# Kernel optimization log

Hardware: AMD Instinct MI355X
Metric: run time of the kernel (lower is better)

The kernel has to match this reference:

```python
import jax, jax.numpy as jnp
import numpy as np

BATCH, NVIS, NHID, NCOND = 4096, 1024, 4096, 512


def setup_inputs() -> dict:
    key = jax.random.key(0)
    ks = jax.random.split(key, 6)
    return {
        "visible_data": jax.random.uniform(ks[0], (BATCH, NVIS), dtype=jnp.float32),
        "cond_data": jax.random.normal(ks[1], (BATCH, NCOND), dtype=jnp.float32),
        # uniform noise replaces torch.bernoulli's internal RNG: sample = (noise < p)
        "noise": jax.random.uniform(ks[2], (BATCH, NHID), dtype=jnp.float32),
        "W": jax.random.normal(ks[3], (NVIS, NHID), dtype=jnp.float32) * 0.1,
        "b": jnp.zeros((1, NVIS), dtype=jnp.float32),
        "c": jnp.zeros((1, NHID), dtype=jnp.float32),
        "A": jax.random.normal(ks[4], (NCOND, NVIS), dtype=jnp.float32) * 0.1,
        "B": jax.random.normal(ks[5], (NCOND, NHID), dtype=jnp.float32) * 0.1,
    }


def reference(visible_data, cond_data, noise, W, b, c, A, B):
    # sample_h_given_vu: sigmoid(v@W + u@B + c), bernoulli sample via uniform noise
    h1_mean = jax.nn.sigmoid(visible_data @ W + cond_data @ B + c)  # [B, nhid]
    h1_sample = (noise < h1_mean).astype(h1_mean.dtype)
    # sample_v_given_hu (binary): L1-normalized exp == softmax, then argmax one-hot
    pre = h1_sample @ W.T + cond_data @ A + b  # [B, nvis]
    v1_mean = jax.nn.softmax(pre, axis=1)
    max_idx = jnp.argmax(v1_mean, axis=1)
    v1_sample = jax.nn.one_hot(max_idx, pre.shape[1], dtype=pre.dtype)
    return v1_sample
```

## Files before the change

kernel.cpp:

```cpp
#include <hip/hip_runtime.h>
#include <math.h>

static constexpr int BATCH = 4096;
static constexpr int NVIS  = 1024;
static constexpr int NHID  = 4096;
static constexpr int NCOND = 512;

typedef __attribute__((ext_vector_type(8))) short bf16x8;
typedef __attribute__((ext_vector_type(4))) float f32x4;

static constexpr unsigned HCAP = 131072;
static constexpr unsigned RCAP = 256;
static constexpr size_t MB = 1u << 20;

static constexpr size_t F_WT0   = 0;
static constexpr size_t F_WT1   = F_WT0  + 8*MB;
static constexpr size_t F_BMT0  = F_WT1  + 8*MB;
static constexpr size_t F_BMT1  = F_BMT0 + 4*MB;
static constexpr size_t F_AT0   = F_BMT1 + 4*MB;
static constexpr size_t F_AT1   = F_AT0  + 1*MB;
static constexpr size_t F_V0    = F_AT1  + 1*MB;
static constexpr size_t F_V1    = F_V0   + 8*MB;
static constexpr size_t F_U0    = F_V1   + 8*MB;
static constexpr size_t F_U1    = F_U0   + 4*MB;
static constexpr size_t F_WR0   = F_U1   + 4*MB;
static constexpr size_t F_WR1   = F_WR0  + 8*MB;
static constexpr size_t F_H     = F_WR1  + 8*MB;
static constexpr size_t F_BB    = F_H    + 32*MB;
static constexpr size_t F_HFLAG = F_BB   + 1*MB;
static constexpr size_t F_RFLAG = F_HFLAG + 512*1024;
static constexpr size_t F_RBEST = F_RFLAG + 16384;
static constexpr size_t F_CNT   = F_RBEST + 16384;
static constexpr size_t F_PREB  = F_CNT  + 256;
static constexpr size_t WS_FULL = F_PREB + 2*MB;

__device__ __forceinline__ void gload16(const void* g, void* l) {
    __builtin_amdgcn_global_load_lds(
        (const __attribute__((address_space(1))) void*)g,
        (__attribute__((address_space(3))) void*)l, 16, 0, 0);
}

__device__ __forceinline__ void split1(float x, unsigned short& hi, unsigned short& lo) {
    unsigned u = __float_as_uint(x);
    unsigned r = u + 0x7FFFu + ((u >> 16) & 1u);
    hi = (unsigned short)(r >> 16);
    float rem = x - __uint_as_float(r & 0xFFFF0000u);
    unsigned u2 = __float_as_uint(rem);
    unsigned r2 = u2 + 0x7FFFu + ((u2 >> 16) & 1u);
    lo = (unsigned short)(r2 >> 16);
}

__device__ __forceinline__ void merge3(float& b, unsigned& ix, float& s,
                                       float b2, unsigned i2, float s2) {
    if (b2 > b || (b2 == b && i2 < ix)) { s = fmaxf(b, s2); b = b2; ix = i2; }
    else                                { s = fmaxf(s, b2); }
}

#define SFENCE() __builtin_amdgcn_sched_barrier(0)
#define BARRIER() do { asm volatile("" ::: "memory"); SFENCE(); \
                       __builtin_amdgcn_s_barrier(); SFENCE(); \
                       asm volatile("" ::: "memory"); } while (0)
#define VMW(N) asm volatile("s_waitcnt vmcnt(" #N ")" ::: "memory")
#define LGKM0() do { asm volatile("s_waitcnt lgkmcnt(0)" ::: "memory"); SFENCE(); } while (0)

__global__ void kz_zero(unsigned* c) { if (threadIdx.x < 64) c[threadIdx.x] = 0; }

__global__ __launch_bounds__(256) void transpose_split(
    const float* __restrict__ src, int R, int C,
    unsigned short* __restrict__ d0, unsigned short* __restrict__ d1) {
    __shared__ float tile[32][33];
    const int c0 = blockIdx.x * 32, r0 = blockIdx.y * 32;
    const int tx = threadIdx.x & 31, ty = threadIdx.x >> 5;
#pragma unroll
    for (int e = 0; e < 4; ++e)
        tile[ty + e * 8][tx] = src[(size_t)(r0 + ty + e * 8) * C + c0 + tx];
    __syncthreads();
#pragma unroll
    for (int e = 0; e < 4; ++e) {
        int c = c0 + ty + e * 8;
        unsigned short hi, lo;
        split1(tile[tx][ty + e * 8], hi, lo);
        d0[(size_t)c * R + r0 + tx] = hi;
        d1[(size_t)c * R + r0 + tx] = lo;
    }
}

__global__ __launch_bounds__(256) void transpose_f32(
    const float* __restrict__ src, int R, int C, float* __restrict__ dst) {
    __shared__ float tile[32][33];
    const int c0 = blockIdx.x * 32, r0 = blockIdx.y * 32;
    const int tx = threadIdx.x & 31, ty = threadIdx.x >> 5;
#pragma unroll
    for (int e = 0; e < 4; ++e)
        tile[ty + e * 8][tx] = src[(size_t)(r0 + ty + e * 8) * C + c0 + tx];
    __syncthreads();
#pragma unroll
    for (int e = 0; e < 4; ++e)
        dst[(size_t)(c0 + ty + e * 8) * R + r0 + tx] = tile[tx][ty + e * 8];
}

__global__ __launch_bounds__(256) void split_planes(
    const float* __restrict__ src, int n4,
    unsigned short* __restrict__ p0, unsigned short* __restrict__ p1) {
    for (int i = blockIdx.x * 256 + threadIdx.x; i < n4; i += gridDim.x * 256) {
        float4 v = ((const float4*)src)[i];
        unsigned short h0,h1,h2,h3,l0,l1,l2,l3;
        split1(v.x,h0,l0); split1(v.y,h1,l1); split1(v.z,h2,l2); split1(v.w,h3,l3);
        ((ushort4*)p0)[i] = make_ushort4(h0,h1,h2,h3);
        ((ushort4*)p1)[i] = make_ushort4(l0,l1,l2,l3);
    }
}

__global__ __launch_bounds__(512, 1) void k1_4p(
    const float* __restrict__ noise,
    const unsigned short* __restrict__ V0, const unsigned short* __restrict__ V1,
    const unsigned short* __restrict__ U0, const unsigned short* __restrict__ U1,
    const unsigned short* __restrict__ WT0, const unsigned short* __restrict__ WT1,
    const unsigned short* __restrict__ BmT0, const unsigned short* __restrict__ BmT1,
    const float* __restrict__ cvec, unsigned short* __restrict__ hout,
    unsigned* __restrict__ hcnt, unsigned* __restrict__ hflag)
{
    __shared__ __align__(16) unsigned short As0[2][256][32], As1[2][256][32],
                                            Bs0[2][256][32], Bs1[2][256][32];
    const int t = threadIdx.x, lane = t & 63, wid = t >> 6;
    const int g = lane >> 4, cc = lane & 15;
    const int wrow = wid >> 2, wcol = wid & 3;
    const int pc = (g ^ ((cc >> 1) & 3)) * 8;
    const int nwg = gridDim.x * gridDim.y;
    const int bid = blockIdx.y * gridDim.x + blockIdx.x;
    const int q = nwg >> 3;
    const int swz = (bid & 7) * q + (bid >> 3);
    const int b0 = (swz / gridDim.x) * 256;
    const int j0 = (swz % gridDim.x) * 256;

    auto srcs = [&](int ks, const unsigned short*& A0_, const unsigned short*& A1_,
                    const unsigned short*& B0_, const unsigned short*& B1_,
                    int& K_, int& k0_) {
        if (ks < 32) { A0_ = V0; A1_ = V1; B0_ = WT0; B1_ = WT1; K_ = 1024; k0_ = ks * 32; }
        else         { A0_ = U0; A1_ = U1; B0_ = BmT0; B1_ = BmT1; K_ = 512; k0_ = (ks - 32) * 32; }
    };
    auto stageA = [&](int ks, int bi, int mh) {
        const unsigned short *A0_, *A1_, *B0_, *B1_; int K_, k0_;
        srcs(ks, A0_, A1_, B0_, B1_, K_, k0_);
        int rl = t >> 2, s = t & 3;
        int r = mh * 128 + rl;
        int sc = s ^ ((r >> 1) & 3);
        size_t ga = (size_t)(b0 + r) * K_ + k0_ + sc * 8;
        size_t ldd = (size_t)mh * 4096 + (size_t)t * 8;
        gload16(A0_ + ga, &As0[bi][0][0] + ldd);
        gload16(A1_ + ga, &As1[bi][0][0] + ldd);
    };
    auto stageB = [&](int ks, int bi, int nh) {
        const unsigned short *A0_, *A1_, *B0_, *B1_; int K_, k0_;
        srcs(ks, A0_, A1_, B0_, B1_, K_, k0_);
        int rl = t >> 2, s = t & 3;
        int r = nh * 128 + rl;
        int sc = s ^ ((r >> 1) & 3);
        size_t gb = (size_t)(j0 + r) * K_ + k0_ + sc * 8;
        size_t ldd = (size_t)nh * 4096 + (size_t)t * 8;
        gload16(B0_ + gb, &Bs0[bi][0][0] + ldd);
        gload16(B1_ + gb, &Bs1[bi][0][0] + ldd);
    };

    f32x4 acc[8][4] = {};
    bf16x8 a0q[4], a1q[4];
    bf16x8 b0a[2][2], b1a[2][2];

    auto readA = [&](int cur, int mh) {
#pragma unroll
        for (int k = 0; k < 4; ++k) {
            int r = wrow * 128 + (4 * mh + k) * 16 + cc;
            a0q[k] = *(const bf16x8*)&As0[cur][r][pc];
            a1q[k] = *(const bf16x8*)&As1[cur][r][pc];
        }
    };
    auto readB = [&](int cur, int nh) {
#pragma unroll
        for (int k = 0; k < 2; ++k) {
            int n = wcol * 64 + (2 * nh + k) * 16 + cc;
            b0a[nh][k] = *(const bf16x8*)&Bs0[cur][n][pc];
            b1a[nh][k] = *(const bf16x8*)&Bs1[cur][n][pc];
        }
    };
    auto mfma24 = [&](int mh, int nh) {
#pragma unroll
        for (int k = 0; k < 4; ++k)
#pragma unroll
            for (int n = 0; n < 2; ++n) {
                f32x4 c = acc[4 * mh + k][2 * nh + n];
                c = __builtin_amdgcn_mfma_f32_16x16x32_bf16(a0q[k], b0a[nh][n], c, 0, 0, 0);
                c = __builtin_amdgcn_mfma_f32_16x16x32_bf16(a0q[k], b1a[nh][n], c, 0, 0, 0);
                c = __builtin_amdgcn_mfma_f32_16x16x32_bf16(a1q[k], b0a[nh][n], c, 0, 0, 0);
                acc[4 * mh + k][2 * nh + n] = c;
            }
    };

    stageA(0, 0, 0);
    stageB(0, 0, 0);
    stageB(0, 0, 1);
    stageA(0, 0, 1);
    VMW(4);
    BARRIER();

    for (int tt = 0; tt < 48; ++tt) {
        const int cur = tt & 1, nb = cur ^ 1;
        const bool pre = (tt + 1 < 48);
        readA(cur, 0); readB(cur, 0);
        if (pre) stageA(tt + 1, nb, 0);
        BARRIER();
        LGKM0();
        __builtin_amdgcn_s_setprio(1); mfma24(0, 0); __builtin_amdgcn_s_setprio(0);
        if (pre) { VMW(4); } else { VMW(2); }
        BARRIER();
        readB(cur, 1);
        if (pre) stageB(tt + 1, nb, 0);
        BARRIER();
        LGKM0();
        __builtin_amdgcn_s_setprio(1); mfma24(0, 1); __builtin_amdgcn_s_setprio(0);
        if (pre) { VMW(4); } else { VMW(0); }
        BARRIER();
        readA(cur, 1);
        if (pre) stageB(tt + 1, nb, 1);
        BARRIER();
        LGKM0();
        __builtin_amdgcn_s_setprio(1); mfma24(1, 0); __builtin_amdgcn_s_setprio(0);
        BARRIER();
        if (pre) stageA(tt + 1, nb, 1);
        BARRIER();
        LGKM0();
        __builtin_amdgcn_s_setprio(1); mfma24(1, 1); __builtin_amdgcn_s_setprio(0);
        if (pre) { VMW(4); }
        BARRIER();
    }

#pragma unroll
    for (int ni = 0; ni < 4; ++ni) {
        int j = j0 + wcol * 64 + ni * 16 + cc;
        float cj = cvec[j];
#pragma unroll
        for (int mi = 0; mi < 8; ++mi) {
#pragma unroll
            for (int i = 0; i < 4; ++i) {
                int b = b0 + wrow * 128 + mi * 16 + g * 4 + i;
                float z = acc[mi][ni][i] + cj;
                float m = 1.0f / (1.0f + __expf(-z));
                float nv = noise[(size_t)b * NHID + j];
                hout[(size_t)b * NHID + j] = (nv < m) ? (unsigned short)0x3F80 : (unsigned short)0;
                if (fabsf(nv - m) < 2.5e-4f) {
                    unsigned p = atomicAdd(hcnt, 1u);
                    if (p < HCAP) hflag[p] = ((unsigned)b << 12) | (unsigned)j;
                }
            }
        }
    }
}

__global__ __launch_bounds__(512, 4) void k2_t(
    const unsigned short* __restrict__ hbf,
    const unsigned short* __restrict__ U0, const unsigned short* __restrict__ U1,
    const unsigned short* __restrict__ WR0, const unsigned short* __restrict__ WR1,
    const unsigned short* __restrict__ AT0, const unsigned short* __restrict__ AT1,
    const float* __restrict__ bvec, float4* __restrict__ blockbest)
{
    __shared__ __align__(16) unsigned short As0[128][32], As1[128][32],
                                            Bs0[128][32], Bs1[128][32];
    __shared__ float4 mbuf[4][128];
    const int t = threadIdx.x, lane = t & 63, wid = t >> 6;
    const int g = lane >> 4, cc = lane & 15;
    const int wrow = wid >> 2, wcol = wid & 3;
    const int pc = (g ^ ((cc >> 1) & 3)) * 8;
    const int nwg = gridDim.x * gridDim.y;
    const int bid = blockIdx.y * gridDim.x + blockIdx.x;
    const int q = nwg >> 3;
    const int swz = (bid & 7) * q + (bid >> 3);
    const int b0 = (swz / gridDim.x) * 128;
    const int i0 = (swz % gridDim.x) * 128;

    f32x4 acc[4][2] = {};

    for (int k0 = 0; k0 < NHID; k0 += 32) {
        __syncthreads();
        {
            int r = t >> 2, s = t & 3, sc = s ^ ((r >> 1) & 3);
            gload16(hbf + (size_t)(b0 + r) * NHID + k0 + sc * 8,
                    &As0[0][0] + (size_t)t * 8);
            size_t go = (size_t)(i0 + r) * NHID + k0 + sc * 8;
            gload16(WR0 + go, &Bs0[0][0] + (size_t)t * 8);
            gload16(WR1 + go, &Bs1[0][0] + (size_t)t * 8);
        }
        __syncthreads();
        bf16x8 bb0[2], bb1[2];
#pragma unroll
        for (int ni = 0; ni < 2; ++ni) {
            int n = wcol * 32 + ni * 16 + cc;
            bb0[ni] = *(const bf16x8*)&Bs0[n][pc];
            bb1[ni] = *(const bf16x8*)&Bs1[n][pc];
        }
#pragma unroll
        for (int mi = 0; mi < 4; ++mi) {
            bf16x8 a = *(const bf16x8*)&As0[wrow * 64 + mi * 16 + cc][pc];
#pragma unroll
            for (int ni = 0; ni < 2; ++ni) {
                acc[mi][ni] = __builtin_amdgcn_mfma_f32_16x16x32_bf16(a, bb0[ni], acc[mi][ni], 0, 0, 0);
                acc[mi][ni] = __builtin_amdgcn_mfma_f32_16x16x32_bf16(a, bb1[ni], acc[mi][ni], 0, 0, 0);
            }
        }
    }
    for (int k0 = 0; k0 < NCOND; k0 += 32) {
        __syncthreads();
        {
            int r = t >> 2, s = t & 3, sc = s ^ ((r >> 1) & 3);
            size_t ga = (size_t)(b0 + r) * NCOND + k0 + sc * 8;
            gload16(U0 + ga, &As0[0][0] + (size_t)t * 8);
            gload16(U1 + ga, &As1[0][0] + (size_t)t * 8);
            size_t go = (size_t)(i0 + r) * NCOND + k0 + sc * 8;
            gload16(AT0 + go, &Bs0[0][0] + (size_t)t * 8);
            gload16(AT1 + go, &Bs1[0][0] + (size_t)t * 8);
        }
        __syncthreads();
        bf16x8 bb0[2], bb1[2];
#pragma unroll
        for (int ni = 0; ni < 2; ++ni) {
            int n = wcol * 32 + ni * 16 + cc;
            bb0[ni] = *(const bf16x8*)&Bs0[n][pc];
            bb1[ni] = *(const bf16x8*)&Bs1[n][pc];
        }
#pragma unroll
        for (int mi = 0; mi < 4; ++mi) {
            int r = wrow * 64 + mi * 16 + cc;
            bf16x8 a0 = *(const bf16x8*)&As0[r][pc];
            bf16x8 a1 = *(const bf16x8*)&As1[r][pc];
#pragma unroll
            for (int ni = 0; ni < 2; ++ni) {
                acc[mi][ni] = __builtin_amdgcn_mfma_f32_16x16x32_bf16(a0, bb0[ni], acc[mi][ni], 0, 0, 0);
                acc[mi][ni] = __builtin_amdgcn_mfma_f32_16x16x32_bf16(a0, bb1[ni], acc[mi][ni], 0, 0, 0);
                acc[mi][ni] = __builtin_amdgcn_mfma_f32_16x16x32_bf16(a1, bb0[ni], acc[mi][ni], 0, 0, 0);
            }
        }
    }

#pragma unroll
    for (int ni = 0; ni < 2; ++ni) {
        int colb = i0 + wcol * 32 + ni * 16 + cc;
        float bb = bvec[colb];
#pragma unroll
        for (int mi = 0; mi < 4; ++mi)
#pragma unroll
            for (int i = 0; i < 4; ++i) acc[mi][ni][i] += bb;
    }
#pragma unroll
    for (int mi = 0; mi < 4; ++mi) {
#pragma unroll
        for (int i = 0; i < 4; ++i) {
            float best = acc[mi][0][i];
            unsigned bidx = (unsigned)(i0 + wcol * 32 + cc);
            float sec = -3.4e38f;
            merge3(best, bidx, sec, acc[mi][1][i],
                   (unsigned)(i0 + wcol * 32 + 16 + cc), -3.4e38f);
#pragma unroll
            for (int m = 1; m < 16; m <<= 1) {
                float ob = __shfl_xor(best, m);
                unsigned oi = __shfl_xor(bidx, m);
                float os = __shfl_xor(sec, m);
                merge3(best, bidx, sec, ob, oi, os);
            }
            if (cc == 0)
                mbuf[wcol][wrow * 64 + mi * 16 + g * 4 + i] =
                    make_float4(best, sec, __uint_as_float(bidx), 0.f);
        }
    }
    __syncthreads();
    if (t < 128) {
        float4 f0 = mbuf[0][t];
        float best = f0.x, sec = f0.y;
        unsigned bidx = __float_as_uint(f0.z);
#pragma unroll
        for (int wq = 1; wq < 4; ++wq) {
            float4 fq = mbuf[wq][t];
            merge3(best, bidx, sec, fq.x, __float_as_uint(fq.z), fq.y);
        }
        blockbest[(size_t)(b0 + t) * 8 + (unsigned)(i0 >> 7)] =
            make_float4(best, sec, __uint_as_float(bidx), 0.f);
    }
}

__global__ __launch_bounds__(256) void k5_recheck_h(
    const float* __restrict__ vd, const float* __restrict__ cd, const float* __restrict__ noise,
    const float* __restrict__ WTf, const float* __restrict__ BmTf, const float* __restrict__ cvec,
    const unsigned* __restrict__ hcnt, const unsigned* __restrict__ hflag,
    unsigned short* __restrict__ h) {
    const int gw = (blockIdx.x * 256 + threadIdx.x) >> 6, lane = threadIdx.x & 63;
    const int nw = gridDim.x * 4;
    unsigned n = *hcnt; if (n > HCAP) n = HCAP;
    for (unsigned e = gw; e < n; e += nw) {
        unsigned p = hflag[e];
        int b = p >> 12, j = p & 4095;
        double s = 0.0;
        for (int k = lane; k < NVIS; k += 64)
            s += (double)vd[(size_t)b * NVIS + k] * (double)WTf[(size_t)j * NVIS + k];
        for (int k = lane; k < NCOND; k += 64)
            s += (double)cd[(size_t)b * NCOND + k] * (double)BmTf[(size_t)j * NCOND + k];
        for (int m = 32; m; m >>= 1) s += __shfl_xor(s, m);
        if (lane == 0) {
            double z = s + (double)cvec[j];
            double mm = 1.0 / (1.0 + exp(-z));
            h[(size_t)b * NHID + j] =
                ((double)noise[(size_t)b * NHID + j] < mm) ? (unsigned short)0x3F80 : (unsigned short)0;
        }
    }
}

__global__ __launch_bounds__(256) void k3_merge8(
    const float4* __restrict__ blockbest, unsigned* __restrict__ rowbest,
    unsigned* __restrict__ rcnt, unsigned* __restrict__ rowflag) {
    const int t = threadIdx.x;
    const int row = blockIdx.x * 32 + (t >> 3), e = t & 7;
    float4 f = blockbest[(size_t)row * 8 + e];
    float best = f.x, sec = f.y;
    unsigned idx = __float_as_uint(f.z);
#pragma unroll
    for (int m = 1; m < 8; m <<= 1) {
        float ob = __shfl_xor(best, m);
        unsigned oi = __shfl_xor(idx, m);
        float os = __shfl_xor(sec, m);
        merge3(best, idx, sec, ob, oi, os);
    }
    if (e == 0) {
        rowbest[row] = idx;
        if (best - sec < 1e-3f) {
            unsigned p = atomicAdd(rcnt, 1u);
            if (p < 4096) rowflag[p] = (unsigned)row;
        }
    }
}

__global__ __launch_bounds__(256) void k_onehot(const unsigned* __restrict__ rowbest,
                                                float* __restrict__ out) {
    const int row = blockIdx.x;
    const unsigned idx = rowbest[row];
    const int base = threadIdx.x * 4;
    float4 o;
    o.x = (base + 0 == (int)idx) ? 1.f : 0.f;
    o.y = (base + 1 == (int)idx) ? 1.f : 0.f;
    o.z = (base + 2 == (int)idx) ? 1.f : 0.f;
    o.w = (base + 3 == (int)idx) ? 1.f : 0.f;
    *(float4*)(out + (size_t)row * NVIS + base) = o;
}

__global__ __launch_bounds__(256) void k6_rows_pre(
    const unsigned short* __restrict__ h, const float* __restrict__ cd,
    const float* __restrict__ W, const float* __restrict__ ATf, const float* __restrict__ bvec,
    const unsigned* __restrict__ rcnt, const unsigned* __restrict__ rowflag,
    double* __restrict__ prebuf) {
    const int gw = (blockIdx.x * 256 + threadIdx.x) >> 6, lane = threadIdx.x & 63;
    const int nw = gridDim.x * 4;
    unsigned n = *rcnt; if (n > RCAP) n = RCAP;
    for (unsigned e = gw; e < n * 1024u; e += nw) {
        int ri = e >> 10, i = e & 1023;
        int b = (int)rowflag[ri];
        double s = 0.0;
        for (int k = lane; k < NHID; k += 64) {
            double hv = h[(size_t)b * NHID + k] ? 1.0 : 0.0;
            s += hv * (double)W[(size_t)i * NHID + k];
        }
        for (int k = lane; k < NCOND; k += 64)
            s += (double)cd[(size_t)b * NCOND + k] * (double)ATf[(size_t)i * NCOND + k];
        for (int m = 32; m; m >>= 1) s += __shfl_xor(s, m);
        if (lane == 0) prebuf[(size_t)ri * 1024 + i] = s + (double)bvec[i];
    }
}

__global__ __launch_bounds__(256) void k6_rows_argmax(
    const unsigned* __restrict__ rcnt, const unsigned* __restrict__ rowflag,
    const double* __restrict__ prebuf, float* __restrict__ out) {
    __shared__ double sv[256];
    __shared__ int si[256];
    unsigned n = *rcnt; if (n > RCAP) n = RCAP;
    const int t = threadIdx.x;
    for (unsigned ri = blockIdx.x; ri < n; ri += gridDim.x) {
        const int row = (int)rowflag[ri];
        const double* pr = prebuf + (size_t)ri * 1024;
        double best = pr[t * 4];
        int bi = t * 4;
#pragma unroll
        for (int e = 1; e < 4; ++e) {
            double v = pr[t * 4 + e];
            if (v > best) { best = v; bi = t * 4 + e; }
        }
        sv[t] = best; si[t] = bi;
        __syncthreads();
        for (int s = 128; s; s >>= 1) {
            if (t < s) {
                double v2 = sv[t + s]; int i2 = si[t + s];
                if (v2 > sv[t] || (v2 == sv[t] && i2 < si[t])) { sv[t] = v2; si[t] = i2; }
            }
            __syncthreads();
        }
        const int amax = si[0];
        const int base = t * 4;
        float4 o;
        o.x = (base + 0 == amax) ? 1.f : 0.f;
        o.y = (base + 1 == amax) ? 1.f : 0.f;
        o.z = (base + 2 == amax) ? 1.f : 0.f;
        o.w = (base + 3 == amax) ? 1.f : 0.f;
        *(float4*)(out + (size_t)row * NVIS + base) = o;
        __syncthreads();
    }
}

extern "C" void kernel_launch(void* const* d_in, const int* in_sizes, int n_in,
                              void* d_out, int out_size, void* d_ws, size_t ws_size,
                              hipStream_t stream) {
    const float* vd = (const float*)d_in[0];
    const float* cd = (const float*)d_in[1];
    const float* nz = (const float*)d_in[2];
    const float* W  = (const float*)d_in[3];
    const float* bv = (const float*)d_in[4];
    const float* cv = (const float*)d_in[5];
    const float* Am = (const float*)d_in[6];
    const float* Bm = (const float*)d_in[7];
    float* out = (float*)d_out;
    char* w = (char*)d_ws;

    unsigned short* WT0  = (unsigned short*)(w + F_WT0);
    unsigned short* WT1  = (unsigned short*)(w + F_WT1);
    unsigned short* BmT0 = (unsigned short*)(w + F_BMT0);
    unsigned short* BmT1 = (unsigned short*)(w + F_BMT1);
    unsigned short* AT0  = (unsigned short*)(w + F_AT0);
    unsigned short* AT1  = (unsigned short*)(w + F_AT1);
    unsigned short* V0   = (unsigned short*)(w + F_V0);
    unsigned short* V1   = (unsigned short*)(w + F_V1);
    unsigned short* U0   = (unsigned short*)(w + F_U0);
    unsigned short* U1   = (unsigned short*)(w + F_U1);
    unsigned short* WR0  = (unsigned short*)(w + F_WR0);
    unsigned short* WR1  = (unsigned short*)(w + F_WR1);
    unsigned short* hbf  = (unsigned short*)(w + F_H);
    float4*   blockbest  = (float4*)(w + F_BB);
    unsigned* hflag      = (unsigned*)(w + F_HFLAG);
    unsigned* rowflag    = (unsigned*)(w + F_RFLAG);
    unsigned* rowbest    = (unsigned*)(w + F_RBEST);
    unsigned* counters   = (unsigned*)(w + F_CNT);
    double*   prebuf     = (double*)(w + F_PREB);
    unsigned* hcnt = &counters[0];
    unsigned* rcnt = &counters[1];
    float* WTf32  = (float*)(w + F_V0);
    float* BmTf32 = (float*)(w + F_WT0);
    float* ATf32  = (float*)(w + F_WT1);

    dim3 blk(256);
    kz_zero<<<1, 64, 0, stream>>>(counters);
    transpose_split<<<dim3(NHID / 32, NVIS / 32), blk, 0, stream>>>(W, NVIS, NHID, WT0, WT1);
    transpose_split<<<dim3(NHID / 32, NCOND / 32), blk, 0, stream>>>(Bm, NCOND, NHID, BmT0, BmT1);
    transpose_split<<<dim3(NVIS / 32, NCOND / 32), blk, 0, stream>>>(Am, NCOND, NVIS, AT0, AT1);
    split_planes<<<2048, blk, 0, stream>>>(vd, BATCH * NVIS / 4, V0, V1);
    split_planes<<<2048, blk, 0, stream>>>(cd, BATCH * NCOND / 4, U0, U1);
    split_planes<<<2048, blk, 0, stream>>>(W, NVIS * NHID / 4, WR0, WR1);
    k1_4p<<<dim3(NHID / 256, BATCH / 256), 512, 0, stream>>>(
        nz, V0, V1, U0, U1, WT0, WT1, BmT0, BmT1, cv, hbf, hcnt, hflag);
    transpose_f32<<<dim3(NHID / 32, NVIS / 32), blk, 0, stream>>>(W, NVIS, NHID, WTf32);
    transpose_f32<<<dim3(NHID / 32, NCOND / 32), blk, 0, stream>>>(Bm, NCOND, NHID, BmTf32);
    transpose_f32<<<dim3(NVIS / 32, NCOND / 32), blk, 0, stream>>>(Am, NCOND, NVIS, ATf32);
    k5_recheck_h<<<256, blk, 0, stream>>>(vd, cd, nz, WTf32, BmTf32, cv, hcnt, hflag, hbf);
    k2_t<<<dim3(NVIS / 128, BATCH / 128), 512, 0, stream>>>(
        hbf, U0, U1, WR0, WR1, AT0, AT1, bv, blockbest);
    k3_merge8<<<BATCH / 32, blk, 0, stream>>>(blockbest, rowbest, rcnt, rowflag);
    k_onehot<<<BATCH, blk, 0, stream>>>(rowbest, out);
    k6_rows_pre<<<512, blk, 0, stream>>>(hbf, cd, W, ATf32, bv, rcnt, rowflag, prebuf);
    k6_rows_argmax<<<64, blk, 0, stream>>>(rcnt, rowflag, prebuf, out);
}
```

Measured before the change: 512.6 us.

## Give each k2 wave a 64x64 tile and fuse W row split into transpose

The second GEMM kernel k2 now runs 256 threads per block with 4 waves in a 2x2 layout instead of 8 waves. Each wave computes a 64x64 output tile, doubling its accumulators, so B fragments are reused across more MFMAs and there is less shared-memory read traffic per flop. The W split into row-major bf16 hi/lo planes is folded into the transpose kernel, which removes one full pass over W. The trade-off is more registers per thread and fewer waves per block, which may hurt latency hiding.

```diff
diff --git a/kernel.cpp b/kernel.cpp
--- a/kernel.cpp
+++ b/kernel.cpp
@@ -82,6 +82,34 @@
         split1(tile[tx][ty + e * 8], hi, lo);
         d0[(size_t)c * R + r0 + tx] = hi;
         d1[(size_t)c * R + r0 + tx] = lo;
+    }
+}
+
+__global__ __launch_bounds__(256) void transpose_split_plus(
+    const float* __restrict__ src, int R, int C,
+    unsigned short* __restrict__ dT0, unsigned short* __restrict__ dT1,
+    unsigned short* __restrict__ dR0, unsigned short* __restrict__ dR1) {
+    __shared__ float tile[32][33];
+    const int c0 = blockIdx.x * 32, r0 = blockIdx.y * 32;
+    const int tx = threadIdx.x & 31, ty = threadIdx.x >> 5;
+#pragma unroll
+    for (int e = 0; e < 4; ++e) {
+        int r = r0 + ty + e * 8;
+        float v = src[(size_t)r * C + c0 + tx];
+        tile[ty + e * 8][tx] = v;
+        unsigned short hi, lo;
+        split1(v, hi, lo);
+        dR0[(size_t)r * C + c0 + tx] = hi;
+        dR1[(size_t)r * C + c0 + tx] = lo;
+    }
+    __syncthreads();
+#pragma unroll
+    for (int e = 0; e < 4; ++e) {
+        int c = c0 + ty + e * 8;
+        unsigned short hi, lo;
+        split1(tile[tx][ty + e * 8], hi, lo);
+        dT0[(size_t)c * R + r0 + tx] = hi;
+        dT1[(size_t)c * R + r0 + tx] = lo;
     }
 }
 
@@ -195,10 +223,7 @@
             }
     };
 
-    stageA(0, 0, 0);
-    stageB(0, 0, 0);
-    stageB(0, 0, 1);
-    stageA(0, 0, 1);
+    stageA(0, 0, 0); stageB(0, 0, 0); stageB(0, 0, 1); stageA(0, 0, 1);
     VMW(4);
     BARRIER();
 
@@ -255,7 +280,7 @@
     }
 }
 
-__global__ __launch_bounds__(512, 4) void k2_t(
+__global__ __launch_bounds__(256, 5) void k2_v(
     const unsigned short* __restrict__ hbf,
     const unsigned short* __restrict__ U0, const unsigned short* __restrict__ U1,
     const unsigned short* __restrict__ WR0, const unsigned short* __restrict__ WR1,
@@ -264,10 +289,10 @@
 {
     __shared__ __align__(16) unsigned short As0[128][32], As1[128][32],
                                             Bs0[128][32], Bs1[128][32];
-    __shared__ float4 mbuf[4][128];
+    __shared__ float4 mbuf[2][128];
     const int t = threadIdx.x, lane = t & 63, wid = t >> 6;
     const int g = lane >> 4, cc = lane & 15;
-    const int wrow = wid >> 2, wcol = wid & 3;
+    const int wrow = wid >> 1, wcol = wid & 1;
     const int pc = (g ^ ((cc >> 1) & 3)) * 8;
     const int nwg = gridDim.x * gridDim.y;
     const int bid = blockIdx.y * gridDim.x + blockIdx.x;
@@ -276,23 +301,28 @@
     const int b0 = (swz / gridDim.x) * 128;
     const int i0 = (swz % gridDim.x) * 128;
 
-    f32x4 acc[4][2] = {};
+    f32x4 acc[4][4] = {};
 
     for (int k0 = 0; k0 < NHID; k0 += 32) {
         __syncthreads();
         {
-            int r = t >> 2, s = t & 3, sc = s ^ ((r >> 1) & 3);
+            int r = t >> 1, s = t & 1;
+        }
+#pragma unroll
+        for (int e = 0; e < 2; ++e) {
+            int idx = t + e * 256, r = idx >> 2, s = idx & 3;
+            int sc = s ^ ((r >> 1) & 3);
             gload16(hbf + (size_t)(b0 + r) * NHID + k0 + sc * 8,
-                    &As0[0][0] + (size_t)t * 8);
+                    &As0[0][0] + (size_t)idx * 8);
             size_t go = (size_t)(i0 + r) * NHID + k0 + sc * 8;
-            gload16(WR0 + go, &Bs0[0][0] + (size_t)t * 8);
-            gload16(WR1 + go, &Bs1[0][0] + (size_t)t * 8);
+            gload16(WR0 + go, &Bs0[0][0] + (size_t)idx * 8);
+            gload16(WR1 + go, &Bs1[0][0] + (size_t)idx * 8);
         }
         __syncthreads();
-        bf16x8 bb0[2], bb1[2];
-#pragma unroll
-        for (int ni = 0; ni < 2; ++ni) {
-            int n = wcol * 32 + ni * 16 + cc;
+        bf16x8 bb0[4], bb1[4];
+#pragma unroll
+        for (int ni = 0; ni < 4; ++ni) {
+            int n = wcol * 64 + ni * 16 + cc;
             bb0[ni] = *(const bf16x8*)&Bs0[n][pc];
             bb1[ni] = *(const bf16x8*)&Bs1[n][pc];
         }
@@ -300,7 +330,7 @@
         for (int mi = 0; mi < 4; ++mi) {
             bf16x8 a = *(const bf16x8*)&As0[wrow * 64 + mi * 16 + cc][pc];
 #pragma unroll
-            for (int ni = 0; ni < 2; ++ni) {
+            for (int ni = 0; ni < 4; ++ni) {
                 acc[mi][ni] = __builtin_amdgcn_mfma_f32_16x16x32_bf16(a, bb0[ni], acc[mi][ni], 0, 0, 0);
                 acc[mi][ni] = __builtin_amdgcn_mfma_f32_16x16x32_bf16(a, bb1[ni], acc[mi][ni], 0, 0, 0);
             }
@@ -308,20 +338,22 @@
     }
     for (int k0 = 0; k0 < NCOND; k0 += 32) {
         __syncthreads();
-        {
-            int r = t >> 2, s = t & 3, sc = s ^ ((r >> 1) & 3);
+#pragma unroll
+        for (int e = 0; e < 2; ++e) {
+            int idx = t + e * 256, r = idx >> 2, s = idx & 3;
+            int sc = s ^ ((r >> 1) & 3);
             size_t ga = (size_t)(b0 + r) * NCOND + k0 + sc * 8;
-            gload16(U0 + ga, &As0[0][0] + (size_t)t * 8);
-            gload16(U1 + ga, &As1[0][0] + (size_t)t * 8);
+            gload16(U0 + ga, &As0[0][0] + (size_t)idx * 8);
+            gload16(U1 + ga, &As1[0][0] + (size_t)idx * 8);
             size_t go = (size_t)(i0 + r) * NCOND + k0 + sc * 8;
-            gload16(AT0 + go, &Bs0[0][0] + (size_t)t * 8);
-            gload16(AT1 + go, &Bs1[0][0] + (size_t)t * 8);
+            gload16(AT0 + go, &Bs0[0][0] + (size_t)idx * 8);
+            gload16(AT1 + go, &Bs1[0][0] + (size_t)idx * 8);
         }
         __syncthreads();
-        bf16x8 bb0[2], bb1[2];
-#pragma unroll
-        for (int ni = 0; ni < 2; ++ni) {
-            int n = wcol * 32 + ni * 16 + cc;
+        bf16x8 bb0[4], bb1[4];
+#pragma unroll
+        for (int ni = 0; ni < 4; ++ni) {
+            int n = wcol * 64 + ni * 16 + cc;
             bb0[ni] = *(const bf16x8*)&Bs0[n][pc];
             bb1[ni] = *(const bf16x8*)&Bs1[n][pc];
         }
@@ -331,7 +363,7 @@
             bf16x8 a0 = *(const bf16x8*)&As0[r][pc];
             bf16x8 a1 = *(const bf16x8*)&As1[r][pc];
 #pragma unroll
-            for (int ni = 0; ni < 2; ++ni) {
+            for (int ni = 0; ni < 4; ++ni) {
                 acc[mi][ni] = __builtin_amdgcn_mfma_f32_16x16x32_bf16(a0, bb0[ni], acc[mi][ni], 0, 0, 0);
                 acc[mi][ni] = __builtin_amdgcn_mfma_f32_16x16x32_bf16(a0, bb1[ni], acc[mi][ni], 0, 0, 0);
                 acc[mi][ni] = __builtin_amdgcn_mfma_f32_16x16x32_bf16(a1, bb0[ni], acc[mi][ni], 0, 0, 0);
@@ -340,8 +372,8 @@
     }
 
 #pragma unroll
-    for (int ni = 0; ni < 2; ++ni) {
-        int colb = i0 + wcol * 32 + ni * 16 + cc;
+    for (int ni = 0; ni < 4; ++ni) {
+        int colb = i0 + wcol * 64 + ni * 16 + cc;
         float bb = bvec[colb];
 #pragma unroll
         for (int mi = 0; mi < 4; ++mi)
@@ -353,10 +385,12 @@
 #pragma unroll
         for (int i = 0; i < 4; ++i) {
             float best = acc[mi][0][i];
-            unsigned bidx = (unsigned)(i0 + wcol * 32 + cc);
+            unsigned bidx = (unsigned)(i0 + wcol * 64 + cc);
             float sec = -3.4e38f;
-            merge3(best, bidx, sec, acc[mi][1][i],
-                   (unsigned)(i0 + wcol * 32 + 16 + cc), -3.4e38f);
+#pragma unroll
+            for (int ni = 1; ni < 4; ++ni)
+                merge3(best, bidx, sec, acc[mi][ni][i],
+                       (unsigned)(i0 + wcol * 64 + ni * 16 + cc), -3.4e38f);
 #pragma unroll
             for (int m = 1; m < 16; m <<= 1) {
                 float ob = __shfl_xor(best, m);
@@ -371,14 +405,10 @@
     }
     __syncthreads();
     if (t < 128) {
-        float4 f0 = mbuf[0][t];
+        float4 f0 = mbuf[0][t], f1 = mbuf[1][t];
         float best = f0.x, sec = f0.y;
         unsigned bidx = __float_as_uint(f0.z);
-#pragma unroll
-        for (int wq = 1; wq < 4; ++wq) {
-            float4 fq = mbuf[wq][t];
-            merge3(best, bidx, sec, fq.x, __float_as_uint(fq.z), fq.y);
-        }
+        merge3(best, bidx, sec, f1.x, __float_as_uint(f1.z), f1.y);
         blockbest[(size_t)(b0 + t) * 8 + (unsigned)(i0 >> 7)] =
             make_float4(best, sec, __uint_as_float(bidx), 0.f);
     }
@@ -549,19 +579,19 @@
 
     dim3 blk(256);
     kz_zero<<<1, 64, 0, stream>>>(counters);
-    transpose_split<<<dim3(NHID / 32, NVIS / 32), blk, 0, stream>>>(W, NVIS, NHID, WT0, WT1);
+    transpose_split_plus<<<dim3(NHID / 32, NVIS / 32), blk, 0, stream>>>(
+        W, NVIS, NHID, WT0, WT1, WR0, WR1);
     transpose_split<<<dim3(NHID / 32, NCOND / 32), blk, 0, stream>>>(Bm, NCOND, NHID, BmT0, BmT1);
     transpose_split<<<dim3(NVIS / 32, NCOND / 32), blk, 0, stream>>>(Am, NCOND, NVIS, AT0, AT1);
     split_planes<<<2048, blk, 0, stream>>>(vd, BATCH * NVIS / 4, V0, V1);
     split_planes<<<2048, blk, 0, stream>>>(cd, BATCH * NCOND / 4, U0, U1);
-    split_planes<<<2048, blk, 0, stream>>>(W, NVIS * NHID / 4, WR0, WR1);
     k1_4p<<<dim3(NHID / 256, BATCH / 256), 512, 0, stream>>>(
         nz, V0, V1, U0, U1, WT0, WT1, BmT0, BmT1, cv, hbf, hcnt, hflag);
     transpose_f32<<<dim3(NHID / 32, NVIS / 32), blk, 0, stream>>>(W, NVIS, NHID, WTf32);
     transpose_f32<<<dim3(NHID / 32, NCOND / 32), blk, 0, stream>>>(Bm, NCOND, NHID, BmTf32);
     transpose_f32<<<dim3(NVIS / 32, NCOND / 32), blk, 0, stream>>>(Am, NCOND, NVIS, ATf32);
     k5_recheck_h<<<256, blk, 0, stream>>>(vd, cd, nz, WTf32, BmTf32, cv, hcnt, hflag, hbf);
-    k2_t<<<dim3(NVIS / 128, BATCH / 128), 512, 0, stream>>>(
+    k2_v<<<dim3(NVIS / 128, BATCH / 128), 256, 0, stream>>>(
         hbf, U0, U1, WR0, WR1, AT0, AT1, bv, blockbest);
     k3_merge8<<<BATCH / 32, blk, 0, stream>>>(blockbest, rowbest, rcnt, rowflag);
     k_onehot<<<BATCH, blk, 0, stream>>>(rowbest, out);
```

After: 525.5 us. 1.03x slower.

## Switch second GEMM to int8 MFMA with two-plane quantized W and byte hidden states

Applied to the files above, without the earlier changes.

Replaces the bf16 split-plane h·Wᵀ GEMM with an int8 path. W is quantized per row into high and low int8 planes with a float scale, and h is stored as bytes. The kernel uses mfma_i32_16x16x64_i8 over K steps of 64 and rescales at the end, which halves the h and W bytes and doubles K per MFMA. The cost is quantization error, absorbed by widening the near-tie threshold that sends rows to the exact fp64 recheck. The occupancy hint also drops from 4 to 2.

```diff
diff --git a/kernel.cpp b/kernel.cpp
--- a/kernel.cpp
+++ b/kernel.cpp
@@ -8,6 +8,7 @@
 
 typedef __attribute__((ext_vector_type(8))) short bf16x8;
 typedef __attribute__((ext_vector_type(4))) float f32x4;
+typedef __attribute__((ext_vector_type(4))) int   i32x4;
 
 static constexpr unsigned HCAP = 131072;
 static constexpr unsigned RCAP = 256;
@@ -23,9 +24,10 @@
 static constexpr size_t F_V1    = F_V0   + 8*MB;
 static constexpr size_t F_U0    = F_V1   + 8*MB;
 static constexpr size_t F_U1    = F_U0   + 4*MB;
-static constexpr size_t F_WR0   = F_U1   + 4*MB;
-static constexpr size_t F_WR1   = F_WR0  + 8*MB;
-static constexpr size_t F_H     = F_WR1  + 8*MB;
+static constexpr size_t F_QH    = F_U1   + 4*MB;
+static constexpr size_t F_QL    = F_QH   + 4*MB;
+static constexpr size_t F_SINV  = F_QL   + 4*MB;
+static constexpr size_t F_H     = F_SINV + 8*MB;
 static constexpr size_t F_BB    = F_H    + 32*MB;
 static constexpr size_t F_HFLAG = F_BB   + 1*MB;
 static constexpr size_t F_RFLAG = F_HFLAG + 512*1024;
@@ -111,13 +113,52 @@
     }
 }
 
+__global__ __launch_bounds__(256) void quantize_w(
+    const float* __restrict__ W, signed char* __restrict__ QH,
+    signed char* __restrict__ QL, float* __restrict__ SINV) {
+    __shared__ float red[256];
+    const int i = blockIdx.x, t = threadIdx.x;
+    const float* row = W + (size_t)i * NHID;
+    float4 v[4];
+    float mx = 0.f;
+#pragma unroll
+    for (int e = 0; e < 4; ++e) {
+        v[e] = *(const float4*)(row + e * 1024 + t * 4);
+        mx = fmaxf(mx, fmaxf(fmaxf(fabsf(v[e].x), fabsf(v[e].y)),
+                             fmaxf(fabsf(v[e].z), fabsf(v[e].w))));
+    }
+    red[t] = mx; __syncthreads();
+    for (int s = 128; s; s >>= 1) {
+        if (t < s) red[t] = fmaxf(red[t], red[t + s]);
+        __syncthreads();
+    }
+    const float rm = fmaxf(red[0], 1e-30f);
+    const float sc = 32256.f / rm;
+    if (t == 0) SINV[i] = rm / 32256.f;
+#pragma unroll
+    for (int e = 0; e < 4; ++e) {
+        const float* pv = (const float*)&v[e];
+        unsigned ph = 0, pl = 0;
+#pragma unroll
+        for (int j = 0; j < 4; ++j) {
+            int wq = (int)lrintf(pv[j] * sc);
+            int hi = (wq + 128) >> 8;
+            int lo = wq - (hi << 8);
+            ph |= ((unsigned)hi & 0xFFu) << (8 * j);
+            pl |= ((unsigned)lo & 0xFFu) << (8 * j);
+        }
+        *(unsigned*)(QH + (size_t)i * NHID + e * 1024 + t * 4) = ph;
+        *(unsigned*)(QL + (size_t)i * NHID + e * 1024 + t * 4) = pl;
+    }
+}
+
 __global__ __launch_bounds__(512, 1) void k1_4p(
     const float* __restrict__ noise,
     const unsigned short* __restrict__ V0, const unsigned short* __restrict__ V1,
     const unsigned short* __restrict__ U0, const unsigned short* __restrict__ U1,
     const unsigned short* __restrict__ WT0, const unsigned short* __restrict__ WT1,
     const unsigned short* __restrict__ BmT0, const unsigned short* __restrict__ BmT1,
-    const float* __restrict__ cvec, unsigned short* __restrict__ hout,
+    const float* __restrict__ cvec, unsigned char* __restrict__ hout,
     unsigned* __restrict__ hcnt, unsigned* __restrict__ hflag)
 {
     __shared__ __align__(16) unsigned short As0[2][256][32], As1[2][256][32],
@@ -195,10 +236,7 @@
             }
     };
 
-    stageA(0, 0, 0);
-    stageB(0, 0, 0);
-    stageB(0, 0, 1);
-    stageA(0, 0, 1);
+    stageA(0, 0, 0); stageB(0, 0, 0); stageB(0, 0, 1); stageA(0, 0, 1);
     VMW(4);
     BARRIER();
 
@@ -245,7 +283,7 @@
                 float z = acc[mi][ni][i] + cj;
                 float m = 1.0f / (1.0f + __expf(-z));
                 float nv = noise[(size_t)b * NHID + j];
-                hout[(size_t)b * NHID + j] = (nv < m) ? (unsigned short)0x3F80 : (unsigned short)0;
+                hout[(size_t)b * NHID + j] = (nv < m) ? (unsigned char)1 : (unsigned char)0;
                 if (fabsf(nv - m) < 2.5e-4f) {
                     unsigned p = atomicAdd(hcnt, 1u);
                     if (p < HCAP) hflag[p] = ((unsigned)b << 12) | (unsigned)j;
@@ -255,20 +293,20 @@
     }
 }
 
-__global__ __launch_bounds__(512, 4) void k2_t(
-    const unsigned short* __restrict__ hbf,
+__global__ __launch_bounds__(512, 2) void k2_i8(
+    const unsigned char* __restrict__ hbf,
     const unsigned short* __restrict__ U0, const unsigned short* __restrict__ U1,
-    const unsigned short* __restrict__ WR0, const unsigned short* __restrict__ WR1,
+    const signed char* __restrict__ QH, const signed char* __restrict__ QL,
+    const float* __restrict__ SINV,
     const unsigned short* __restrict__ AT0, const unsigned short* __restrict__ AT1,
     const float* __restrict__ bvec, float4* __restrict__ blockbest)
 {
-    __shared__ __align__(16) unsigned short As0[128][32], As1[128][32],
-                                            Bs0[128][32], Bs1[128][32];
+    __shared__ __align__(16) char smem[32768];
     __shared__ float4 mbuf[4][128];
     const int t = threadIdx.x, lane = t & 63, wid = t >> 6;
     const int g = lane >> 4, cc = lane & 15;
     const int wrow = wid >> 2, wcol = wid & 3;
-    const int pc = (g ^ ((cc >> 1) & 3)) * 8;
+    const int pcb = (g ^ ((cc >> 1) & 3)) * 16;
     const int nwg = gridDim.x * gridDim.y;
     const int bid = blockIdx.y * gridDim.x + blockIdx.x;
     const int q = nwg >> 3;
@@ -276,60 +314,80 @@
     const int b0 = (swz / gridDim.x) * 128;
     const int i0 = (swz % gridDim.x) * 128;
 
-    f32x4 acc[4][2] = {};
-
-    for (int k0 = 0; k0 < NHID; k0 += 32) {
+    char* Ah  = smem;
+    char* Qhs = smem + 8192;
+    char* Qls = smem + 16384;
+
+    i32x4 ah[4][2] = {}, al[4][2] = {};
+
+    for (int k0 = 0; k0 < NHID; k0 += 64) {
         __syncthreads();
         {
             int r = t >> 2, s = t & 3, sc = s ^ ((r >> 1) & 3);
-            gload16(hbf + (size_t)(b0 + r) * NHID + k0 + sc * 8,
-                    &As0[0][0] + (size_t)t * 8);
-            size_t go = (size_t)(i0 + r) * NHID + k0 + sc * 8;
-            gload16(WR0 + go, &Bs0[0][0] + (size_t)t * 8);
-            gload16(WR1 + go, &Bs1[0][0] + (size_t)t * 8);
+            size_t off = (size_t)r * 64 + s * 16;
+            gload16(hbf + (size_t)(b0 + r) * NHID + k0 + sc * 16, Ah + off);
+            gload16(QH + (size_t)(i0 + r) * NHID + k0 + sc * 16, Qhs + off);
+            gload16(QL + (size_t)(i0 + r) * NHID + k0 + sc * 16, Qls + off);
         }
         __syncthreads();
-        bf16x8 bb0[2], bb1[2];
+        i32x4 bh[2], bl[2];
 #pragma unroll
         for (int ni = 0; ni < 2; ++ni) {
             int n = wcol * 32 + ni * 16 + cc;
-            bb0[ni] = *(const bf16x8*)&Bs0[n][pc];
-            bb1[ni] = *(const bf16x8*)&Bs1[n][pc];
+            bh[ni] = *(const i32x4*)(Qhs + (size_t)n * 64 + pcb);
+            bl[ni] = *(const i32x4*)(Qls + (size_t)n * 64 + pcb);
         }
 #pragma unroll
         for (int mi = 0; mi < 4; ++mi) {
-            bf16x8 a = *(const bf16x8*)&As0[wrow * 64 + mi * 16 + cc][pc];
+            i32x4 a = *(const i32x4*)(Ah + (size_t)(wrow * 64 + mi * 16 + cc) * 64 + pcb);
 #pragma unroll
             for (int ni = 0; ni < 2; ++ni) {
-                acc[mi][ni] = __builtin_amdgcn_mfma_f32_16x16x32_bf16(a, bb0[ni], acc[mi][ni], 0, 0, 0);
-                acc[mi][ni] = __builtin_amdgcn_mfma_f32_16x16x32_bf16(a, bb1[ni], acc[mi][ni], 0, 0, 0);
+                ah[mi][ni] = __builtin_amdgcn_mfma_i32_16x16x64_i8(a, bh[ni], ah[mi][ni], 0, 0, 0);
+                al[mi][ni] = __builtin_amdgcn_mfma_i32_16x16x64_i8(a, bl[ni], al[mi][ni], 0, 0, 0);
             }
         }
     }
+    f32x4 acc[4][2];
+#pragma unroll
+    for (int ni = 0; ni < 2; ++ni) {
+        int col = i0 + wcol * 32 + ni * 16 + cc;
+        float sv = SINV[col];
+#pragma unroll
+        for (int mi = 0; mi < 4; ++mi)
+#pragma unroll
+            for (int e = 0; e < 4; ++e)
+                acc[mi][ni][e] = fmaf(256.f, (float)ah[mi][ni][e], (float)al[mi][ni][e]) * sv;
+    }
+
+    char* As0 = smem;
+    char* As1 = smem + 8192;
+    char* Bs0 = smem + 16384;
+    char* Bs1 = smem + 24576;
     for (int k0 = 0; k0 < NCOND; k0 += 32) {
         __syncthreads();
         {
             int r = t >> 2, s = t & 3, sc = s ^ ((r >> 1) & 3);
+            size_t off = (size_t)r * 64 + s * 16;
             size_t ga = (size_t)(b0 + r) * NCOND + k0 + sc * 8;
-            gload16(U0 + ga, &As0[0][0] + (size_t)t * 8);
-            gload16(U1 + ga, &As1[0][0] + (size_t)t * 8);
+            gload16(U0 + ga, As0 + off);
+            gload16(U1 + ga, As1 + off);
             size_t go = (size_t)(i0 + r) * NCOND + k0 + sc * 8;
-            gload16(AT0 + go, &Bs0[0][0] + (size_t)t * 8);
-            gload16(AT1 + go, &Bs1[0][0] + (size_t)t * 8);
+            gload16(AT0 + go, Bs0 + off);
+            gload16(AT1 + go, Bs1 + off);
         }
         __syncthreads();
         bf16x8 bb0[2], bb1[2];
 #pragma unroll
         for (int ni = 0; ni < 2; ++ni) {
             int n = wcol * 32 + ni * 16 + cc;
-            bb0[ni] = *(const bf16x8*)&Bs0[n][pc];
-            bb1[ni] = *(const bf16x8*)&Bs1[n][pc];
+            bb0[ni] = *(const bf16x8*)(Bs0 + (size_t)n * 64 + pcb);
+            bb1[ni] = *(const bf16x8*)(Bs1 + (size_t)n * 64 + pcb);
         }
 #pragma unroll
         for (int mi = 0; mi < 4; ++mi) {
             int r = wrow * 64 + mi * 16 + cc;
-            bf16x8 a0 = *(const bf16x8*)&As0[r][pc];
-            bf16x8 a1 = *(const bf16x8*)&As1[r][pc];
+            bf16x8 a0 = *(const bf16x8*)(As0 + (size_t)r * 64 + pcb);
+            bf16x8 a1 = *(const bf16x8*)(As1 + (size_t)r * 64 + pcb);
 #pragma unroll
             for (int ni = 0; ni < 2; ++ni) {
                 acc[mi][ni] = __builtin_amdgcn_mfma_f32_16x16x32_bf16(a0, bb0[ni], acc[mi][ni], 0, 0, 0);
@@ -388,7 +446,7 @@
     const float* __restrict__ vd, const float* __restrict__ cd, const float* __restrict__ noise,
     const float* __restrict__ WTf, const float* __restrict__ BmTf, const float* __restrict__ cvec,
     const unsigned* __restrict__ hcnt, const unsigned* __restrict__ hflag,
-    unsigned short* __restrict__ h) {
+    unsigned char* __restrict__ h) {
     const int gw = (blockIdx.x * 256 + threadIdx.x) >> 6, lane = threadIdx.x & 63;
     const int nw = gridDim.x * 4;
     unsigned n = *hcnt; if (n > HCAP) n = HCAP;
@@ -405,7 +463,7 @@
             double z = s + (double)cvec[j];
             double mm = 1.0 / (1.0 + exp(-z));
             h[(size_t)b * NHID + j] =
-                ((double)noise[(size_t)b * NHID + j] < mm) ? (unsigned short)0x3F80 : (unsigned short)0;
+                ((double)noise[(size_t)b * NHID + j] < mm) ? (unsigned char)1 : (unsigned char)0;
         }
     }
 }
@@ -427,7 +485,7 @@
     }
     if (e == 0) {
         rowbest[row] = idx;
-        if (best - sec < 1e-3f) {
+        if (best - sec < 4e-3f) {
             unsigned p = atomicAdd(rcnt, 1u);
             if (p < 4096) rowflag[p] = (unsigned)row;
         }
@@ -448,7 +506,7 @@
 }
 
 __global__ __launch_bounds__(256) void k6_rows_pre(
-    const unsigned short* __restrict__ h, const float* __restrict__ cd,
+    const unsigned char* __restrict__ h, const float* __restrict__ cd,
     const float* __restrict__ W, const float* __restrict__ ATf, const float* __restrict__ bvec,
     const unsigned* __restrict__ rcnt, const unsigned* __restrict__ rowflag,
     double* __restrict__ prebuf) {
@@ -532,9 +590,10 @@
     unsigned short* V1   = (unsigned short*)(w + F_V1);
     unsigned short* U0   = (unsigned short*)(w + F_U0);
     unsigned short* U1   = (unsigned short*)(w + F_U1);
-    unsigned short* WR0  = (unsigned short*)(w + F_WR0);
-    unsigned short* WR1  = (unsigned short*)(w + F_WR1);
-    unsigned short* hbf  = (unsigned short*)(w + F_H);
+    signed char*    QH   = (signed char*)(w + F_QH);
+    signed char*    QL   = (signed char*)(w + F_QL);
+    float*          SINV = (float*)(w + F_SINV);
+    unsigned char*  hbf  = (unsigned char*)(w + F_H);
     float4*   blockbest  = (float4*)(w + F_BB);
     unsigned* hflag      = (unsigned*)(w + F_HFLAG);
     unsigned* rowflag    = (unsigned*)(w + F_RFLAG);
@@ -554,15 +613,15 @@
     transpose_split<<<dim3(NVIS / 32, NCOND / 32), blk, 0, stream>>>(Am, NCOND, NVIS, AT0, AT1);
     split_planes<<<2048, blk, 0, stream>>>(vd, BATCH * NVIS / 4, V0, V1);
     split_planes<<<2048, blk, 0, stream>>>(cd, BATCH * NCOND / 4, U0, U1);
-    split_planes<<<2048, blk, 0, stream>>>(W, NVIS * NHID / 4, WR0, WR1);
+    quantize_w<<<NVIS, blk, 0, stream>>>(W, QH, QL, SINV);
     k1_4p<<<dim3(NHID / 256, BATCH / 256), 512, 0, stream>>>(
         nz, V0, V1, U0, U1, WT0, WT1, BmT0, BmT1, cv, hbf, hcnt, hflag);
     transpose_f32<<<dim3(NHID / 32, NVIS / 32), blk, 0, stream>>>(W, NVIS, NHID, WTf32);
     transpose_f32<<<dim3(NHID / 32, NCOND / 32), blk, 0, stream>>>(Bm, NCOND, NHID, BmTf32);
     transpose_f32<<<dim3(NVIS / 32, NCOND / 32), blk, 0, stream>>>(Am, NCOND, NVIS, ATf32);
     k5_recheck_h<<<256, blk, 0, stream>>>(vd, cd, nz, WTf32, BmTf32, cv, hcnt, hflag, hbf);
-    k2_t<<<dim3(NVIS / 128, BATCH / 128), 512, 0, stream>>>(
-        hbf, U0, U1, WR0, WR1, AT0, AT1, bv, blockbest);
+    k2_i8<<<dim3(NVIS / 128, BATCH / 128), 512, 0, stream>>>(
+        hbf, U0, U1, QH, QL, SINV, AT0, AT1, bv, blockbest);
     k3_merge8<<<BATCH / 32, blk, 0, stream>>>(blockbest, rowbest, rcnt, rowflag);
     k_onehot<<<BATCH, blk, 0, stream>>>(rowbest, out);
     k6_rows_pre<<<512, blk, 0, stream>>>(hbf, cd, W, ATf32, bv, rcnt, rowflag, prebuf);
```

New measurement: 512.9 us. No clear change (+0.1%).
